# Kernel optimization log

Measured on AMD Instinct MI355X. Metric: run time of the kernel, lower is better.

## Reference

```python
import jax, jax.numpy as jnp
import numpy as np

D_MODEL = 1024
N_EXPERTS = 8
HIDDEN = ((int(round(D_MODEL * (8.0 / 3.0))) + 63) // 64) * 64  # 2752
ALPHA = 0.05  # load_balance_alpha


def setup_inputs() -> dict:
    key = jax.random.key(0)
    ks = jax.random.split(key, 6)
    s = 0.02
    x = jax.random.normal(ks[0], (4, 1024, D_MODEL), dtype=jnp.float32)
    Wg = jax.random.normal(ks[1], (D_MODEL, N_EXPERTS), dtype=jnp.float32) * s
    bg = jnp.zeros((N_EXPERTS,), dtype=jnp.float32)
    Wu = jax.random.normal(ks[2], (N_EXPERTS, D_MODEL, HIDDEN), dtype=jnp.float32) * s
    Wv = jax.random.normal(ks[3], (N_EXPERTS, D_MODEL, HIDDEN), dtype=jnp.float32) * s
    Wd = jax.random.normal(ks[4], (N_EXPERTS, HIDDEN, D_MODEL), dtype=jnp.float32) * s
    return {"x": x, "Wg": Wg, "bg": bg, "Wu": Wu, "Wv": Wv, "Wd": Wd}


def reference(x, Wg, bg, Wu, Wv, Wd):
    b, t, d = x.shape
    E = Wu.shape[0]
    xf = x.reshape(b * t, d)  # [N, d]

    # Top-1 router
    logits = xf @ Wg + bg                      # [N, E]
    probs = jax.nn.softmax(logits, axis=-1)
    top1_idx = jnp.argmax(probs, axis=-1)      # [N]
    top1_p = jnp.max(probs, axis=-1)           # [N]
    onehot = jax.nn.one_hot(top1_idx, E, dtype=x.dtype)  # [N, E]

    # Load-balancing aux loss (both me and ce are under no_grad in the original)
    me = jax.lax.stop_gradient(onehot.mean(axis=0))
    ce = jax.lax.stop_gradient(probs.mean(axis=0))
    aux = ALPHA * E * jnp.sum(me * ce)

    # Dropless dispatch: masked per-expert SwiGLU (loop over small fixed E)
    gate = onehot * top1_p[:, None]            # [N, E] combine weights
    y = jnp.zeros_like(xf)
    for e in range(E):
        u = xf @ Wu[e]                         # [N, H]
        v = xf @ Wv[e]                         # [N, H]
        ye = (jax.nn.silu(u) * v) @ Wd[e]      # [N, d]
        y = y + gate[:, e, None] * ye

    return y.reshape(b, t, d), aux
```

## Files before the change

kernel.cpp:

```cpp
#include <hip/hip_runtime.h>

#define D_MODEL 1024
#define HID     2752
#define NEXP    8
#define NTOK    4096
#define ALPHA   0.05f

typedef __bf16 bf16_t;
typedef bf16_t bf16x8 __attribute__((ext_vector_type(8)));
typedef float  f32x4  __attribute__((ext_vector_type(4)));

__device__ inline unsigned short f2bf(float f) {
    unsigned int u = __float_as_uint(f);
    u += 0x7fffu + ((u >> 16) & 1u);
    return (unsigned short)(u >> 16);
}

__device__ inline bf16x8 ldsFrag(const unsigned short* p) {
    union { uint4 u; bf16x8 b; } t;
    t.u = *(const uint4*)p;
    return t.b;
}

__device__ inline void gload_lds16(const void* g, void* l) {
    __builtin_amdgcn_global_load_lds((const __attribute__((address_space(1))) void*)g,
                                     (__attribute__((address_space(3))) void*)l, 16, 0, 0);
}

__global__ void tobf16_kernel(const float* __restrict__ x, unsigned short* __restrict__ xbf) {
    int i = (blockIdx.x * 256 + threadIdx.x) * 8;
    float4 a = *(const float4*)(x + i);
    float4 b = *(const float4*)(x + i + 4);
    uint4 o;
    o.x = (unsigned)f2bf(a.x) | ((unsigned)f2bf(a.y) << 16);
    o.y = (unsigned)f2bf(a.z) | ((unsigned)f2bf(a.w) << 16);
    o.z = (unsigned)f2bf(b.x) | ((unsigned)f2bf(b.y) << 16);
    o.w = (unsigned)f2bf(b.z) | ((unsigned)f2bf(b.w) << 16);
    *(uint4*)(xbf + i) = o;
}

__global__ __launch_bounds__(256) void transposeUV_kernel(const float* __restrict__ Wu,
                                                          const float* __restrict__ Wv,
                                                          unsigned short* __restrict__ WuT,
                                                          unsigned short* __restrict__ WvT) {
    __shared__ float tile[64 * 65];
    const int z = blockIdx.z;
    const int e = z & 7;
    const float* src = ((z < 8) ? Wu : Wv) + (size_t)e * D_MODEL * HID;
    unsigned short* dst = ((z < 8) ? WuT : WvT) + (size_t)e * D_MODEL * HID;
    const int c0 = blockIdx.x * 64, r0 = blockIdx.y * 64;
    const int tid = threadIdx.x;
#pragma unroll
    for (int j = 0; j < 4; ++j) {
        int f = j * 256 + tid;
        int row = f >> 4, c4 = f & 15;
        float4 v = *(const float4*)(src + (size_t)(r0 + row) * HID + c0 + c4 * 4);
        float* t = &tile[row * 65 + c4 * 4];
        t[0] = v.x; t[1] = v.y; t[2] = v.z; t[3] = v.w;
    }
    __syncthreads();
#pragma unroll
    for (int j = 0; j < 2; ++j) {
        int f = j * 256 + tid;
        int orow = f >> 3, kc = f & 7;
        unsigned short pk[8];
#pragma unroll
        for (int q = 0; q < 8; ++q) pk[q] = f2bf(tile[(kc * 8 + q) * 65 + orow]);
        *(uint4*)(dst + (size_t)(c0 + orow) * D_MODEL + r0 + kc * 8) = *(uint4*)pk;
    }
}

__global__ __launch_bounds__(256) void transpose_kernel(const float* __restrict__ in,
                                                        unsigned short* __restrict__ out,
                                                        int R, int C) {
    __shared__ float tile[64 * 65];
    const int e = blockIdx.z;
    const float* src = in + (size_t)e * R * C;
    unsigned short* dst = out + (size_t)e * R * C;
    const int c0 = blockIdx.x * 64, r0 = blockIdx.y * 64;
    const int tid = threadIdx.x;
#pragma unroll
    for (int j = 0; j < 4; ++j) {
        int f = j * 256 + tid;
        int row = f >> 4, c4 = f & 15;
        float4 v = *(const float4*)(src + (size_t)(r0 + row) * C + c0 + c4 * 4);
        float* t = &tile[row * 65 + c4 * 4];
        t[0] = v.x; t[1] = v.y; t[2] = v.z; t[3] = v.w;
    }
    __syncthreads();
#pragma unroll
    for (int j = 0; j < 2; ++j) {
        int f = j * 256 + tid;
        int orow = f >> 3, kc = f & 7;
        unsigned short pk[8];
#pragma unroll
        for (int q = 0; q < 8; ++q) pk[q] = f2bf(tile[(kc * 8 + q) * 65 + orow]);
        *(uint4*)(dst + (size_t)(c0 + orow) * R + r0 + kc * 8) = *(uint4*)pk;
    }
}

__global__ void router_kernel(const float* __restrict__ x, const float* __restrict__ Wg,
                              const float* __restrict__ bg,
                              int* __restrict__ eidx, float* __restrict__ gate_p,
                              int* __restrict__ counts, float* __restrict__ ce_sum) {
    __shared__ float ceS[8];
    __shared__ int   cntS[8];
    int tid = threadIdx.x;
    if (tid < 8) { ceS[tid] = 0.f; cntS[tid] = 0; }
    __syncthreads();

    int wid = tid >> 6, lane = tid & 63;
    int t = blockIdx.x * 16 + wid;
    const float* xr = x + (size_t)t * D_MODEL;

    float acc[8];
#pragma unroll
    for (int e = 0; e < 8; ++e) acc[e] = 0.f;

#pragma unroll
    for (int c = 0; c < 4; ++c) {
        int i0 = c * 256 + lane * 4;
        float4 xv = *(const float4*)(xr + i0);
#pragma unroll
        for (int j = 0; j < 4; ++j) {
            const float* wr = Wg + (size_t)(i0 + j) * 8;
            float4 lo = *(const float4*)(wr);
            float4 hi = *(const float4*)(wr + 4);
            float xs = (&xv.x)[j];
            acc[0] += xs * lo.x; acc[1] += xs * lo.y;
            acc[2] += xs * lo.z; acc[3] += xs * lo.w;
            acc[4] += xs * hi.x; acc[5] += xs * hi.y;
            acc[6] += xs * hi.z; acc[7] += xs * hi.w;
        }
    }
#pragma unroll
    for (int e = 0; e < 8; ++e) {
#pragma unroll
        for (int off = 32; off > 0; off >>= 1)
            acc[e] += __shfl_xor(acc[e], off, 64);
    }

    if (lane == 0) {
        float lg[8];
#pragma unroll
        for (int e = 0; e < 8; ++e) lg[e] = acc[e] + bg[e];
        float mx = lg[0]; int am = 0;
#pragma unroll
        for (int e = 1; e < 8; ++e) { if (lg[e] > mx) { mx = lg[e]; am = e; } }
        float ex[8], s = 0.f;
#pragma unroll
        for (int e = 0; e < 8; ++e) { ex[e] = __expf(lg[e] - mx); s += ex[e]; }
        float inv = 1.f / s;
#pragma unroll
        for (int e = 0; e < 8; ++e) atomicAdd(&ceS[e], ex[e] * inv);
        atomicAdd(&cntS[am], 1);
        eidx[t] = am;
        gate_p[t] = ex[am] * inv;
    }
    __syncthreads();
    if (tid < 8) atomicAdd(&ce_sum[tid], ceS[tid]);
    if (tid >= 8 && tid < 16) atomicAdd(&counts[tid - 8], cntS[tid - 8]);
}

__global__ void offsets_aux_kernel(const int* __restrict__ counts, const float* __restrict__ ce_sum,
                                   int* __restrict__ offs, float* __restrict__ aux_out) {
    if (threadIdx.x == 0) {
        int off = 0; float aux = 0.f;
        for (int e = 0; e < 8; ++e) {
            offs[e] = off; off += counts[e];
            aux += ((float)counts[e] / (float)NTOK) * (ce_sum[e] / (float)NTOK);
        }
        aux_out[0] = ALPHA * (float)NEXP * aux;
    }
}

__global__ void scatter_kernel(const int* __restrict__ eidx, const int* __restrict__ offs,
                               int* __restrict__ fill, int* __restrict__ toks) {
    int t = blockIdx.x * 256 + threadIdx.x;
    int e = eidx[t];
    int pos = atomicAdd(&fill[e], 1);
    toks[offs[e] + pos] = t;
}

__global__ __launch_bounds__(256, 2) void gemm1_kernel(
    const unsigned short* __restrict__ WuT, const unsigned short* __restrict__ WvT,
    const unsigned short* __restrict__ xbf,
    const int* __restrict__ toks, const int* __restrict__ counts, const int* __restrict__ offs,
    unsigned short* __restrict__ hbuf) {
    const int e = blockIdx.z;
    const int Ne = counts[e];
    const int mt = blockIdx.y;
    if (mt * 128 >= Ne) return;
    const int nt = blockIdx.x;
    const int slot0 = offs[e] + mt * 128;
    const int rowsV = min(128, Ne - mt * 128);
    const int ncol0 = nt * 128;
    const int colsV = min(128, HID - ncol0);

    __shared__ unsigned short As[128 * 64];
    __shared__ unsigned short Bus[128 * 64];
    __shared__ unsigned short Bvs[128 * 64];

    const int tid = threadIdx.x;

    const unsigned short* aS[4];
    const unsigned short* buS[4];
    const unsigned short* bvS[4];
    unsigned short* aD[4];
    unsigned short* buD[4];
    unsigned short* bvD[4];
#pragma unroll
    for (int i = 0; i < 4; ++i) {
        int c = i * 256 + tid;
        int r = c >> 3, ch = c & 7;
        int srcOff = ((ch ^ (r & 7)) * 8);
        int ar = min(r, rowsV - 1);
        int tok = toks[slot0 + ar];
        aS[i] = xbf + (size_t)tok * D_MODEL + srcOff;
        int bn = ncol0 + min(r, colsV - 1);
        buS[i] = WuT + ((size_t)e * HID + bn) * D_MODEL + srcOff;
        bvS[i] = WvT + ((size_t)e * HID + bn) * D_MODEL + srcOff;
        aD[i]  = As  + c * 8;
        buD[i] = Bus + c * 8;
        bvD[i] = Bvs + c * 8;
    }

    f32x4 accU[4][4], accV[4][4];
#pragma unroll
    for (int m = 0; m < 4; ++m)
#pragma unroll
        for (int n = 0; n < 4; ++n) {
            accU[m][n] = (f32x4){0.f, 0.f, 0.f, 0.f};
            accV[m][n] = (f32x4){0.f, 0.f, 0.f, 0.f};
        }

    const int lane = tid & 63;
    const int w = tid >> 6;
    const int rbase = (w >> 1) * 64;
    const int cbase = (w & 1) * 64;
    const int lrow = lane & 15;
    const int lchunk = lane >> 4;

    for (int ks = 0; ks < 16; ++ks) {
#pragma unroll
        for (int i = 0; i < 4; ++i) gload_lds16(aS[i],  aD[i]);
#pragma unroll
        for (int i = 0; i < 4; ++i) gload_lds16(buS[i], buD[i]);
#pragma unroll
        for (int i = 0; i < 4; ++i) gload_lds16(bvS[i], bvD[i]);
#pragma unroll
        for (int i = 0; i < 4; ++i) { aS[i] += 64; buS[i] += 64; bvS[i] += 64; }
        __syncthreads();

#pragma unroll
        for (int kk = 0; kk < 2; ++kk) {
            const int g = kk * 4 + lchunk;
            bf16x8 af[4], bu[4], bv[4];
#pragma unroll
            for (int m = 0; m < 4; ++m) {
                int r = rbase + m * 16 + lrow;
                af[m] = ldsFrag(&As[r * 64 + ((g ^ (r & 7)) * 8)]);
            }
#pragma unroll
            for (int n = 0; n < 4; ++n) {
                int rn = cbase + n * 16 + lrow;
                int off = rn * 64 + ((g ^ (rn & 7)) * 8);
                bu[n] = ldsFrag(&Bus[off]);
                bv[n] = ldsFrag(&Bvs[off]);
            }
#pragma unroll
            for (int m = 0; m < 4; ++m)
#pragma unroll
                for (int n = 0; n < 4; ++n) {
                    accU[m][n] = __builtin_amdgcn_mfma_f32_16x16x32_bf16(af[m], bu[n], accU[m][n], 0, 0, 0);
                    accV[m][n] = __builtin_amdgcn_mfma_f32_16x16x32_bf16(af[m], bv[n], accV[m][n], 0, 0, 0);
                }
        }
        __syncthreads();
    }

#pragma unroll
    for (int m = 0; m < 4; ++m) {
#pragma unroll
        for (int i = 0; i < 4; ++i) {
            int r = rbase + m * 16 + (lane >> 4) * 4 + i;
            if (r >= rowsV) continue;
            size_t rowOff = (size_t)(slot0 + r) * HID + ncol0;
#pragma unroll
            for (int n = 0; n < 4; ++n) {
                int c = cbase + n * 16 + (lane & 15);
                if (c < colsV) {
                    float u = accU[m][n][i];
                    float v = accV[m][n][i];
                    float s = u / (1.f + __expf(-u));
                    hbuf[rowOff + c] = f2bf(s * v);
                }
            }
        }
    }
}

__global__ __launch_bounds__(256, 2) void gemm2_kernel(
    const unsigned short* __restrict__ WdT, const unsigned short* __restrict__ hbuf,
    const int* __restrict__ toks, const int* __restrict__ counts, const int* __restrict__ offs,
    const float* __restrict__ gate_p, float* __restrict__ yout) {
    const int e = blockIdx.z;
    const int Ne = counts[e];
    const int mt = blockIdx.y;
    if (mt * 128 >= Ne) return;
    const int nt = blockIdx.x;
    const int slot0 = offs[e] + mt * 128;
    const int rowsV = min(128, Ne - mt * 128);
    const int ncol0 = nt * 64;

    __shared__ unsigned short As[128 * 64];
    __shared__ unsigned short Bs[64 * 64];

    const int tid = threadIdx.x;

    const unsigned short* aS[4];
    unsigned short* aD[4];
#pragma unroll
    for (int i = 0; i < 4; ++i) {
        int c = i * 256 + tid;
        int r = c >> 3, ch = c & 7;
        int srcOff = ((ch ^ (r & 7)) * 8);
        int ar = min(r, rowsV - 1);
        aS[i] = hbuf + (size_t)(slot0 + ar) * HID + srcOff;
        aD[i] = As + c * 8;
    }
    const unsigned short* bS[2];
    unsigned short* bD[2];
#pragma unroll
    for (int i = 0; i < 2; ++i) {
        int c = i * 256 + tid;
        int r = c >> 3, ch = c & 7;
        int srcOff = ((ch ^ (r & 7)) * 8);
        bS[i] = WdT + ((size_t)e * D_MODEL + ncol0 + r) * HID + srcOff;
        bD[i] = Bs + c * 8;
    }

    f32x4 acc[4][2];
#pragma unroll
    for (int m = 0; m < 4; ++m)
#pragma unroll
        for (int n = 0; n < 2; ++n) acc[m][n] = (f32x4){0.f, 0.f, 0.f, 0.f};

    const int lane = tid & 63;
    const int w = tid >> 6;
    const int rbase = (w >> 1) * 64;
    const int cbase = (w & 1) * 32;
    const int lrow = lane & 15;
    const int lchunk = lane >> 4;

    for (int ks = 0; ks < 43; ++ks) {
#pragma unroll
        for (int i = 0; i < 4; ++i) gload_lds16(aS[i], aD[i]);
#pragma unroll
        for (int i = 0; i < 2; ++i) gload_lds16(bS[i], bD[i]);
#pragma unroll
        for (int i = 0; i < 4; ++i) aS[i] += 64;
#pragma unroll
        for (int i = 0; i < 2; ++i) bS[i] += 64;
        __syncthreads();

#pragma unroll
        for (int kk = 0; kk < 2; ++kk) {
            const int g = kk * 4 + lchunk;
            bf16x8 af[4], bf[2];
#pragma unroll
            for (int m = 0; m < 4; ++m) {
                int r = rbase + m * 16 + lrow;
                af[m] = ldsFrag(&As[r * 64 + ((g ^ (r & 7)) * 8)]);
            }
#pragma unroll
            for (int n = 0; n < 2; ++n) {
                int rn = cbase + n * 16 + lrow;
                bf[n] = ldsFrag(&Bs[rn * 64 + ((g ^ (rn & 7)) * 8)]);
            }
#pragma unroll
            for (int m = 0; m < 4; ++m)
#pragma unroll
                for (int n = 0; n < 2; ++n)
                    acc[m][n] = __builtin_amdgcn_mfma_f32_16x16x32_bf16(af[m], bf[n], acc[m][n], 0, 0, 0);
        }
        __syncthreads();
    }

#pragma unroll
    for (int m = 0; m < 4; ++m) {
#pragma unroll
        for (int i = 0; i < 4; ++i) {
            int r = rbase + m * 16 + (lane >> 4) * 4 + i;
            if (r >= rowsV) continue;
            int tok = toks[slot0 + r];
            float p = gate_p[tok];
            float* yrow = yout + (size_t)tok * D_MODEL + ncol0;
#pragma unroll
            for (int n = 0; n < 2; ++n) {
                int c = cbase + n * 16 + (lane & 15);
                yrow[c] = p * acc[m][n][i];
            }
        }
    }
}

extern "C" void kernel_launch(void* const* d_in, const int* in_sizes, int n_in,
                              void* d_out, int out_size, void* d_ws, size_t ws_size,
                              hipStream_t stream) {
    const float* x  = (const float*)d_in[0];
    const float* Wg = (const float*)d_in[1];
    const float* bg = (const float*)d_in[2];
    const float* Wu = (const float*)d_in[3];
    const float* Wv = (const float*)d_in[4];
    const float* Wd = (const float*)d_in[5];
    float* yout = (float*)d_out;
    float* aux_out = yout + (size_t)NTOK * D_MODEL;

    char* ws = (char*)d_ws;
    int*   counts = (int*)(ws + 0);
    int*   offs   = (int*)(ws + 32);
    float* ce_sum = (float*)(ws + 64);
    int*   fill   = (int*)(ws + 96);
    int*   eidx   = (int*)(ws + 128);
    float* gate_p = (float*)(ws + 16512);
    int*   toks   = (int*)(ws + 32896);
    unsigned short* xbf  = (unsigned short*)(ws + 65536);
    unsigned short* hbuf = (unsigned short*)(ws + 8454144);
    unsigned short* WuT  = (unsigned short*)(ws + 30998528);
    unsigned short* WvT  = (unsigned short*)(ws + 76087296);
    unsigned short* WdT  = WuT;

    hipMemsetAsync(ws, 0, 128, stream);
    tobf16_kernel<<<2048, 256, 0, stream>>>(x, xbf);
    router_kernel<<<256, 1024, 0, stream>>>(x, Wg, bg, eidx, gate_p, counts, ce_sum);
    offsets_aux_kernel<<<1, 64, 0, stream>>>(counts, ce_sum, offs, aux_out);
    scatter_kernel<<<16, 256, 0, stream>>>(eidx, offs, fill, toks);
    transposeUV_kernel<<<dim3(HID / 64, D_MODEL / 64, 16), 256, 0, stream>>>(Wu, Wv, WuT, WvT);
    gemm1_kernel<<<dim3(22, 32, 8), 256, 0, stream>>>(WuT, WvT, xbf, toks, counts, offs, hbuf);
    transpose_kernel<<<dim3(D_MODEL / 64, HID / 64, 8), 256, 0, stream>>>(Wd, WdT, HID, D_MODEL);
    gemm2_kernel<<<dim3(16, 32, 8), 256, 0, stream>>>(WdT, hbuf, toks, counts, offs, gate_p, yout);
}
```

Measured before the change: 279.5 us.

## Fuse bf16 cast into router, co-schedule Wd transpose with gemm1, double-buffer gemm2

Folds the x-to-bf16 conversion into the router kernel so x is read once and one launch is dropped. Appends the Wd transpose blocks to the gemm1 grid when the workspace is large enough, so the transpose runs concurrently with gemm1 instead of as a separate serial launch. Flattens both GEMM grids with the expert index in the low bits. Double-buffers the gemm2 LDS tiles with MFMA priority hints to overlap global loads with compute. This adds LDS use in gemm2 and needs extra workspace for a separate WdT buffer.

```diff
diff --git a/kernel.cpp b/kernel.cpp
--- a/kernel.cpp
+++ b/kernel.cpp
@@ -6,6 +6,9 @@
 #define NTOK    4096
 #define ALPHA   0.05f
 
+#define G1_BLOCKS (8 * 32 * 22)
+#define WDT_TILES (16 * 43 * 8)
+
 typedef __bf16 bf16_t;
 typedef bf16_t bf16x8 __attribute__((ext_vector_type(8)));
 typedef float  f32x4  __attribute__((ext_vector_type(4)));
@@ -25,18 +28,6 @@
 __device__ inline void gload_lds16(const void* g, void* l) {
     __builtin_amdgcn_global_load_lds((const __attribute__((address_space(1))) void*)g,
                                      (__attribute__((address_space(3))) void*)l, 16, 0, 0);
-}
-
-__global__ void tobf16_kernel(const float* __restrict__ x, unsigned short* __restrict__ xbf) {
-    int i = (blockIdx.x * 256 + threadIdx.x) * 8;
-    float4 a = *(const float4*)(x + i);
-    float4 b = *(const float4*)(x + i + 4);
-    uint4 o;
-    o.x = (unsigned)f2bf(a.x) | ((unsigned)f2bf(a.y) << 16);
-    o.y = (unsigned)f2bf(a.z) | ((unsigned)f2bf(a.w) << 16);
-    o.z = (unsigned)f2bf(b.x) | ((unsigned)f2bf(b.y) << 16);
-    o.w = (unsigned)f2bf(b.z) | ((unsigned)f2bf(b.w) << 16);
-    *(uint4*)(xbf + i) = o;
 }
 
 __global__ __launch_bounds__(256) void transposeUV_kernel(const float* __restrict__ Wu,
@@ -102,7 +93,8 @@
 __global__ void router_kernel(const float* __restrict__ x, const float* __restrict__ Wg,
                               const float* __restrict__ bg,
                               int* __restrict__ eidx, float* __restrict__ gate_p,
-                              int* __restrict__ counts, float* __restrict__ ce_sum) {
+                              int* __restrict__ counts, float* __restrict__ ce_sum,
+                              unsigned short* __restrict__ xbf) {
     __shared__ float ceS[8];
     __shared__ int   cntS[8];
     int tid = threadIdx.x;
@@ -112,6 +104,7 @@
     int wid = tid >> 6, lane = tid & 63;
     int t = blockIdx.x * 16 + wid;
     const float* xr = x + (size_t)t * D_MODEL;
+    unsigned short* xbr = xbf + (size_t)t * D_MODEL;
 
     float acc[8];
 #pragma unroll
@@ -121,6 +114,10 @@
     for (int c = 0; c < 4; ++c) {
         int i0 = c * 256 + lane * 4;
         float4 xv = *(const float4*)(xr + i0);
+        uint2 pk;
+        pk.x = (unsigned)f2bf(xv.x) | ((unsigned)f2bf(xv.y) << 16);
+        pk.y = (unsigned)f2bf(xv.z) | ((unsigned)f2bf(xv.w) << 16);
+        *(uint2*)(xbr + i0) = pk;
 #pragma unroll
         for (int j = 0; j < 4; ++j) {
             const float* wr = Wg + (size_t)(i0 + j) * 8;
@@ -186,22 +183,58 @@
     const unsigned short* __restrict__ WuT, const unsigned short* __restrict__ WvT,
     const unsigned short* __restrict__ xbf,
     const int* __restrict__ toks, const int* __restrict__ counts, const int* __restrict__ offs,
-    unsigned short* __restrict__ hbuf) {
-    const int e = blockIdx.z;
+    unsigned short* __restrict__ hbuf,
+    const float* __restrict__ Wd, unsigned short* __restrict__ WdT) {
+
+    __shared__ __align__(16) unsigned char ldsbuf[48 * 1024];
+    unsigned short* As  = (unsigned short*)ldsbuf;
+    unsigned short* Bus = (unsigned short*)(ldsbuf + 16384);
+    unsigned short* Bvs = (unsigned short*)(ldsbuf + 32768);
+
+    const int id = blockIdx.x;
+    const int tid = threadIdx.x;
+
+    if (id >= G1_BLOCKS) {
+        const int t  = id - G1_BLOCKS;
+        const int xt = t & 15;
+        const int rr = t >> 4;
+        const int yt = rr % 43;
+        const int e2 = rr / 43;
+        const float* src = Wd + (size_t)e2 * HID * D_MODEL;
+        unsigned short* dst = WdT + (size_t)e2 * HID * D_MODEL;
+        const int c0 = xt * 64, r0 = yt * 64;
+        float* tile = (float*)ldsbuf;
+#pragma unroll
+        for (int j = 0; j < 4; ++j) {
+            int f = j * 256 + tid;
+            int row = f >> 4, c4 = f & 15;
+            float4 v = *(const float4*)(src + (size_t)(r0 + row) * D_MODEL + c0 + c4 * 4);
+            float* tp = &tile[row * 65 + c4 * 4];
+            tp[0] = v.x; tp[1] = v.y; tp[2] = v.z; tp[3] = v.w;
+        }
+        __syncthreads();
+#pragma unroll
+        for (int j = 0; j < 2; ++j) {
+            int f = j * 256 + tid;
+            int orow = f >> 3, kc = f & 7;
+            unsigned short pk[8];
+#pragma unroll
+            for (int q = 0; q < 8; ++q) pk[q] = f2bf(tile[(kc * 8 + q) * 65 + orow]);
+            *(uint4*)(dst + (size_t)(c0 + orow) * HID + r0 + kc * 8) = *(uint4*)pk;
+        }
+        return;
+    }
+
+    const int e  = id & 7;
+    const int j  = id >> 3;
+    const int mt = j & 31;
+    const int nt = j >> 5;
     const int Ne = counts[e];
-    const int mt = blockIdx.y;
     if (mt * 128 >= Ne) return;
-    const int nt = blockIdx.x;
     const int slot0 = offs[e] + mt * 128;
     const int rowsV = min(128, Ne - mt * 128);
     const int ncol0 = nt * 128;
     const int colsV = min(128, HID - ncol0);
-
-    __shared__ unsigned short As[128 * 64];
-    __shared__ unsigned short Bus[128 * 64];
-    __shared__ unsigned short Bvs[128 * 64];
-
-    const int tid = threadIdx.x;
 
     const unsigned short* aS[4];
     const unsigned short* buS[4];
@@ -300,44 +333,83 @@
     }
 }
 
+
+#define G2_STAGE(AS, BS)                                                  \
+    {                                                                     \
+        _Pragma("unroll")                                                 \
+        for (int i = 0; i < 4; ++i) { gload_lds16(aS[i], &AS[aOff[i]]); aS[i] += 64; } \
+        _Pragma("unroll")                                                 \
+        for (int i = 0; i < 2; ++i) { gload_lds16(bS[i], &BS[bOff[i]]); bS[i] += 64; } \
+    }
+
+#define G2_COMPUTE(AS, BS)                                                \
+    {                                                                     \
+        _Pragma("unroll")                                                 \
+        for (int kk = 0; kk < 2; ++kk) {                                  \
+            const int g = kk * 4 + lchunk;                                \
+            bf16x8 af[4], bf[2];                                          \
+            _Pragma("unroll")                                             \
+            for (int m = 0; m < 4; ++m) {                                 \
+                int r = rbase + m * 16 + lrow;                            \
+                af[m] = ldsFrag(&AS[r * 64 + ((g ^ (r & 7)) * 8)]);       \
+            }                                                             \
+            _Pragma("unroll")                                             \
+            for (int n = 0; n < 2; ++n) {                                 \
+                int rn = cbase + n * 16 + lrow;                           \
+                bf[n] = ldsFrag(&BS[rn * 64 + ((g ^ (rn & 7)) * 8)]);     \
+            }                                                             \
+            __builtin_amdgcn_s_setprio(1);                                \
+            _Pragma("unroll")                                             \
+            for (int m = 0; m < 4; ++m)                                   \
+                _Pragma("unroll")                                         \
+                for (int n = 0; n < 2; ++n)                               \
+                    acc[m][n] = __builtin_amdgcn_mfma_f32_16x16x32_bf16(af[m], bf[n], acc[m][n], 0, 0, 0); \
+            __builtin_amdgcn_s_setprio(0);                                \
+        }                                                                 \
+    }
+
 __global__ __launch_bounds__(256, 2) void gemm2_kernel(
     const unsigned short* __restrict__ WdT, const unsigned short* __restrict__ hbuf,
     const int* __restrict__ toks, const int* __restrict__ counts, const int* __restrict__ offs,
     const float* __restrict__ gate_p, float* __restrict__ yout) {
-    const int e = blockIdx.z;
+    const int id = blockIdx.x;
+    const int e  = id & 7;
+    const int j  = id >> 3;
+    const int mt = j & 31;
+    const int nt = j >> 5;
     const int Ne = counts[e];
-    const int mt = blockIdx.y;
     if (mt * 128 >= Ne) return;
-    const int nt = blockIdx.x;
     const int slot0 = offs[e] + mt * 128;
     const int rowsV = min(128, Ne - mt * 128);
     const int ncol0 = nt * 64;
 
-    __shared__ unsigned short As[128 * 64];
-    __shared__ unsigned short Bs[64 * 64];
+    __shared__ unsigned short As0[128 * 64];
+    __shared__ unsigned short As1[128 * 64];
+    __shared__ unsigned short Bs0[64 * 64];
+    __shared__ unsigned short Bs1[64 * 64];
 
     const int tid = threadIdx.x;
 
     const unsigned short* aS[4];
-    unsigned short* aD[4];
+    int aOff[4];
 #pragma unroll
     for (int i = 0; i < 4; ++i) {
         int c = i * 256 + tid;
         int r = c >> 3, ch = c & 7;
-        int srcOff = ((ch ^ (r & 7)) * 8);
+        int srcOff = (ch ^ (r & 7)) * 8;
         int ar = min(r, rowsV - 1);
         aS[i] = hbuf + (size_t)(slot0 + ar) * HID + srcOff;
-        aD[i] = As + c * 8;
+        aOff[i] = c * 8;
     }
     const unsigned short* bS[2];
-    unsigned short* bD[2];
+    int bOff[2];
 #pragma unroll
     for (int i = 0; i < 2; ++i) {
         int c = i * 256 + tid;
         int r = c >> 3, ch = c & 7;
-        int srcOff = ((ch ^ (r & 7)) * 8);
+        int srcOff = (ch ^ (r & 7)) * 8;
         bS[i] = WdT + ((size_t)e * D_MODEL + ncol0 + r) * HID + srcOff;
-        bD[i] = Bs + c * 8;
+        bOff[i] = c * 8;
     }
 
     f32x4 acc[4][2];
@@ -353,39 +425,19 @@
     const int lrow = lane & 15;
     const int lchunk = lane >> 4;
 
-    for (int ks = 0; ks < 43; ++ks) {
-#pragma unroll
-        for (int i = 0; i < 4; ++i) gload_lds16(aS[i], aD[i]);
-#pragma unroll
-        for (int i = 0; i < 2; ++i) gload_lds16(bS[i], bD[i]);
-#pragma unroll
-        for (int i = 0; i < 4; ++i) aS[i] += 64;
-#pragma unroll
-        for (int i = 0; i < 2; ++i) bS[i] += 64;
+    G2_STAGE(As0, Bs0);
+    __syncthreads();
+
+#pragma unroll 1
+    for (int k2 = 0; k2 < 21; ++k2) {
+        G2_STAGE(As1, Bs1);
+        G2_COMPUTE(As0, Bs0);
         __syncthreads();
-
-#pragma unroll
-        for (int kk = 0; kk < 2; ++kk) {
-            const int g = kk * 4 + lchunk;
-            bf16x8 af[4], bf[2];
-#pragma unroll
-            for (int m = 0; m < 4; ++m) {
-                int r = rbase + m * 16 + lrow;
-                af[m] = ldsFrag(&As[r * 64 + ((g ^ (r & 7)) * 8)]);
-            }
-#pragma unroll
-            for (int n = 0; n < 2; ++n) {
-                int rn = cbase + n * 16 + lrow;
-                bf[n] = ldsFrag(&Bs[rn * 64 + ((g ^ (rn & 7)) * 8)]);
-            }
-#pragma unroll
-            for (int m = 0; m < 4; ++m)
-#pragma unroll
-                for (int n = 0; n < 2; ++n)
-                    acc[m][n] = __builtin_amdgcn_mfma_f32_16x16x32_bf16(af[m], bf[n], acc[m][n], 0, 0, 0);
-        }
+        G2_STAGE(As0, Bs0);
+        G2_COMPUTE(As1, Bs1);
         __syncthreads();
     }
+    G2_COMPUTE(As0, Bs0);
 
 #pragma unroll
     for (int m = 0; m < 4; ++m) {
@@ -429,15 +481,19 @@
     unsigned short* hbuf = (unsigned short*)(ws + 8454144);
     unsigned short* WuT  = (unsigned short*)(ws + 30998528);
     unsigned short* WvT  = (unsigned short*)(ws + 76087296);
-    unsigned short* WdT  = WuT;
+    const size_t WDT_OFF = 121176064;
+    const size_t WDT_SZ  = (size_t)NEXP * D_MODEL * HID * 2;
+    const bool fused = ws_size >= WDT_OFF + WDT_SZ;
+    unsigned short* WdT = fused ? (unsigned short*)(ws + WDT_OFF) : WuT;
 
     hipMemsetAsync(ws, 0, 128, stream);
-    tobf16_kernel<<<2048, 256, 0, stream>>>(x, xbf);
-    router_kernel<<<256, 1024, 0, stream>>>(x, Wg, bg, eidx, gate_p, counts, ce_sum);
+    router_kernel<<<256, 1024, 0, stream>>>(x, Wg, bg, eidx, gate_p, counts, ce_sum, xbf);
     offsets_aux_kernel<<<1, 64, 0, stream>>>(counts, ce_sum, offs, aux_out);
     scatter_kernel<<<16, 256, 0, stream>>>(eidx, offs, fill, toks);
     transposeUV_kernel<<<dim3(HID / 64, D_MODEL / 64, 16), 256, 0, stream>>>(Wu, Wv, WuT, WvT);
-    gemm1_kernel<<<dim3(22, 32, 8), 256, 0, stream>>>(WuT, WvT, xbf, toks, counts, offs, hbuf);
-    transpose_kernel<<<dim3(D_MODEL / 64, HID / 64, 8), 256, 0, stream>>>(Wd, WdT, HID, D_MODEL);
-    gemm2_kernel<<<dim3(16, 32, 8), 256, 0, stream>>>(WdT, hbuf, toks, counts, offs, gate_p, yout);
-}
+    gemm1_kernel<<<fused ? (G1_BLOCKS + WDT_TILES) : G1_BLOCKS, 256, 0, stream>>>(
+        WuT, WvT, xbf, toks, counts, offs, hbuf, Wd, WdT);
+    if (!fused)
+        transpose_kernel<<<dim3(D_MODEL / 64, HID / 64, 8), 256, 0, stream>>>(Wd, WdT, HID, D_MODEL);
+    gemm2_kernel<<<8 * 32 * 16, 256, 0, stream>>>(WdT, hbuf, toks, counts, offs, gate_p, yout);
+}
```

Result: faster. 266.1 us (-4.8%).
